# Kernel optimization log

Measured on AMD Instinct MI355X. Metric: run time of the kernel, lower is better.

Reference implementation:

```python
import jax, jax.numpy as jnp
import numpy as np

B, N, H, DH, E, D_IN = 2, 2048, 8, 32, 65536, 256
O = H * DH
SCALE = float(np.sqrt(DH))


def setup_inputs() -> dict:
    key = jax.random.key(0)
    ks = jax.random.split(key, 8)
    rng = np.random.default_rng(0)
    x = jax.random.normal(ks[0], (B, N, D_IN), jnp.float32)
    adj = jax.random.uniform(ks[1], (B, N, N), jnp.float32)
    # unique edges per graph so scatter-add matches torch advanced-index +=
    flat = np.stack([rng.choice(N * N, size=E, replace=False) for _ in range(B)])
    edge_index = jnp.asarray(np.stack([flat // N, flat % N], axis=1), jnp.int32)  # [B,2,E]
    edge_attr = jax.random.normal(ks[2], (B, E, H), jnp.float32)
    mask = jnp.ones((B, N), dtype=bool)
    qkv_w = jax.random.normal(ks[3], (D_IN, 3 * O), jnp.float32) / np.sqrt(D_IN)
    qkv_b = jnp.zeros((3 * O,), jnp.float32)
    e_w1 = jax.random.normal(ks[4], (H, H), jnp.float32) / np.sqrt(H)
    e_b1 = jnp.zeros((H,), jnp.float32)
    e_w2 = jax.random.normal(ks[5], (H, H), jnp.float32) / np.sqrt(H)
    e_b2 = jnp.zeros((H,), jnp.float32)
    shifts = jnp.asarray(np.linspace(0.1, 0.8, H), jnp.float32).reshape(1, H, 1, 1)
    widths = jnp.full((1, H, 1, 1), 0.5, jnp.float32)
    self_loop_W = jnp.asarray(1.0 / DH + rng.uniform(0, 1, H), jnp.float32).reshape(1, H, 1, 1)
    return dict(x=x, adj=adj, edge_attr=edge_attr, qkv_w=qkv_w, qkv_b=qkv_b,
                e_w1=e_w1, e_b1=e_b1, e_w2=e_w2, e_b2=e_b2,
                shifts=shifts, widths=widths, self_loop_W=self_loop_W,
                edge_index=edge_index, mask=mask)


def reference(x, adj, edge_attr, qkv_w, qkv_b, e_w1, e_b1, e_w2, e_b2,
              shifts, widths, self_loop_W, edge_index, mask):
    Bq, Nq = x.shape[0], x.shape[1]
    # qkv projection -> [3,B,H,N,DH]
    qkv = (x @ qkv_w + qkv_b).reshape(Bq, Nq, 3, H, DH)
    qkv = jnp.transpose(qkv, (2, 0, 3, 1, 4))
    Q, K, V = qkv[0], qkv[1], qkv[2]
    # edge FFN applied twice (eval mode: noise/dropout are identity)
    def ffn(e):
        return jax.nn.relu(e @ e_w1 + e_b1) @ e_w2 + e_b2
    ea = ffn(ffn(edge_attr))                      # [B,E,H]
    ea = jnp.transpose(ea, (0, 2, 1))             # [B,H,E]
    # scores + learned moire adjacency bias
    scores = jnp.einsum('bhqd,bhkd->bhqk', Q, K) / SCALE
    moire = jnp.exp(-((adj[:, None] - shifts) ** 2) / (2.0 * widths ** 2))  # gaussian focus
    moire = jnp.clip(moire, 1e-6, None)
    s = scores + jnp.log(moire)                   # [B,H,N,N]
    # scatter edge features into score matrix
    u = edge_index[:, 0, :]                        # [B,E]
    v = edge_index[:, 1, :]
    bi = jnp.arange(Bq)[:, None, None]
    hi = jnp.arange(H)[None, :, None]
    s = s.at[bi, hi, u[:, None, :], v[:, None, :]].add(ea)
    # self-loop diagonal bias (non-trainable)
    s = s + jnp.eye(Nq, dtype=s.dtype)[None, None] * self_loop_W
    # mask and softmax
    m2 = mask[:, None, :] & mask[:, :, None]       # [B,N,N]
    s = jnp.where(m2[:, None], s, jnp.asarray(-1e6, s.dtype))
    attn = jax.nn.softmax(s, axis=-1)
    out = jnp.einsum('bhqk,bhkd->bhqd', attn, V)
    return jnp.transpose(out, (0, 2, 1, 3)).reshape(Bq, Nq, O)
```

## Files before the change

kernel.cpp:

```cpp
#include <hip/hip_runtime.h>

#define B_ 2
#define N_ 2048
#define H_ 8
#define DH_ 32
#define E_ 65536
#define DIN_ 256
#define KT 256
#define PAD 4
#define ECAP 32
#define INV_SCALE 0.17677669529663687f
#define LOGMIN -13.815510557964274f

typedef short bf16x8 __attribute__((ext_vector_type(8)));
typedef float floatx4 __attribute__((ext_vector_type(4)));

__device__ __forceinline__ unsigned short f2b(float f){
  union { float f; unsigned int u; } v; v.f = f;
  return (unsigned short)((v.u + 0x7fffu + ((v.u >> 16) & 1u)) >> 16);
}
__device__ __forceinline__ bf16x8 f8_to_bf(const float* p){
  float4 a = *(const float4*)p, b = *(const float4*)(p + 4);
  bf16x8 r;
  r[0] = (short)f2b(a.x); r[1] = (short)f2b(a.y); r[2] = (short)f2b(a.z); r[3] = (short)f2b(a.w);
  r[4] = (short)f2b(b.x); r[5] = (short)f2b(b.y); r[6] = (short)f2b(b.z); r[7] = (short)f2b(b.w);
  return r;
}

__global__ __launch_bounds__(256) void prep_kernel(
    const float* __restrict__ eattr,
    const float* __restrict__ w1, const float* __restrict__ b1,
    const float* __restrict__ w2, const float* __restrict__ b2,
    float* __restrict__ ea,
    const int* __restrict__ ei, int* __restrict__ cnt, unsigned int* __restrict__ pck,
    const float* __restrict__ w, unsigned short* __restrict__ wT)
{
  int bb = blockIdx.x, tid = threadIdx.x;
  if (bb < 512){
    __shared__ float W1[64], W2[64], Bv1[8], Bv2[8];
    if (tid < 64){ W1[tid] = w1[tid]; W2[tid] = w2[tid]; }
    if (tid < 8){ Bv1[tid] = b1[tid]; Bv2[tid] = b2[tid]; }
    __syncthreads();
    int gid = bb * 256 + tid;
    const float* ep = eattr + (size_t)gid * 8;
    float cur[8];
#pragma unroll
    for (int i = 0; i < 8; ++i) cur[i] = ep[i];
#pragma unroll
    for (int pass = 0; pass < 2; ++pass){
      float t[8];
#pragma unroll
      for (int j = 0; j < 8; ++j){
        float s = Bv1[j];
#pragma unroll
        for (int i = 0; i < 8; ++i) s += cur[i] * W1[i * 8 + j];
        t[j] = fmaxf(s, 0.f);
      }
#pragma unroll
      for (int j = 0; j < 8; ++j){
        float s = Bv2[j];
#pragma unroll
        for (int i = 0; i < 8; ++i) s += t[i] * W2[i * 8 + j];
        cur[j] = s;
      }
    }
    float* op = ea + (size_t)gid * 8;
#pragma unroll
    for (int j = 0; j < 8; ++j) op[j] = cur[j];
  } else if (bb < 1024){
    int gid = (bb - 512) * 256 + tid;
    int b = gid >> 16, e = gid & (E_ - 1);
    int u = ei[(size_t)b * 2 * E_ + e];
    int v = ei[(size_t)b * 2 * E_ + E_ + e];
    int bucket = ((b << 11) + u) * 8 + (v >> 8);
    int slot = atomicAdd(&cnt[bucket], 1);
    if (slot < ECAP) pck[(size_t)bucket * ECAP + slot] = ((unsigned int)e << 11) | (unsigned int)v;
  } else {
    int k = bb - 1024;
    for (int c = tid; c < 768; c += 256)
      wT[(size_t)c * 256 + k] = f2b(w[(size_t)k * 768 + c]);
  }
}

__global__ __launch_bounds__(256) void qkv_kernel(
    const float* __restrict__ x, const unsigned short* __restrict__ wT,
    const float* __restrict__ bias,
    unsigned short* __restrict__ Qb, unsigned short* __restrict__ Kb, unsigned short* __restrict__ Vt)
{
  int tid = threadIdx.x;
  int wave = tid >> 6, lane = tid & 63, m = lane & 15, quad = lane >> 4;
  int rowbase = blockIdx.x * 16;
  int colbase = blockIdx.y * 64 + wave * 16;
  floatx4 acc = {0.f, 0.f, 0.f, 0.f};
#pragma unroll
  for (int kb = 0; kb < 8; ++kb){
    bf16x8 af = f8_to_bf(x + (size_t)(rowbase + m) * DIN_ + kb * 32 + quad * 8);
    bf16x8 bf = *(const bf16x8*)(wT + (size_t)(colbase + m) * DIN_ + kb * 32 + quad * 8);
    acc = __builtin_amdgcn_mfma_f32_16x16x32_bf16(af, bf, acc, 0, 0, 0);
  }
  int ccol = colbase + m;
  int which = ccol >> 8, hh = (ccol >> 5) & 7, dh = ccol & 31;
  float bv = bias[ccol];
#pragma unroll
  for (int r = 0; r < 4; ++r){
    int row = rowbase + quad * 4 + r;
    int bidx = row >> 11, n = row & (N_ - 1);
    float val = acc[r] + bv;
    size_t bh = (size_t)(bidx * H_ + hh);
    if (which == 0)      Qb[(bh * N_ + n) * DH_ + dh] = f2b(val * INV_SCALE);
    else if (which == 1) Kb[(bh * N_ + n) * DH_ + dh] = f2b(val);
    else                 Vt[(bh * DH_ + dh) * N_ + n] = f2b(val);
  }
}

__global__ __launch_bounds__(256) void attn_kernel(
    const unsigned short* __restrict__ Qb, const unsigned short* __restrict__ Kb,
    const unsigned short* __restrict__ Vt, const float* __restrict__ adj,
    const float* __restrict__ ea, const int* __restrict__ cnt, const unsigned int* __restrict__ pck,
    const float* __restrict__ shifts, const float* __restrict__ widths,
    const float* __restrict__ selfW, float* __restrict__ out)
{
  __shared__ float S[16][KT + PAD];
  __shared__ float mpart[4][16];
  __shared__ float mrowW[4][16];
  __shared__ float arowW[4][16];
  __shared__ float lfin[4][16];

  int bid = blockIdx.x;
  int qt = bid & 127, h = (bid >> 7) & 7, b = bid >> 10;
  int qbase = qt * 16;
  int tid = threadIdx.x, wave = tid >> 6, lane = tid & 63, m = lane & 15, quad = lane >> 4;
  float shift_h = shifts[h];
  float w_h = widths[h];
  float i2w_h = 1.f / (2.f * w_h * w_h);
  float selfW_h = selfW[h];
  size_t krow = (size_t)(b * H_ + h) * N_;
  size_t vrow = (size_t)(b * H_ + h) * DH_;
  bf16x8 qfrag = *(const bf16x8*)(Qb + (krow + qbase + m) * DH_ + quad * 8);

  float mcur = -1e30f;
  float lcur = 0.f;
  floatx4 oacc0 = {0.f, 0.f, 0.f, 0.f};
  floatx4 oacc1 = {0.f, 0.f, 0.f, 0.f};

  for (int kt = 0; kt < N_ / KT; ++kt){
    int k0 = kt * KT;
    bool diagtile = (k0 == (qbase & ~(KT - 1)));
#pragma unroll
    for (int s = 0; s < 4; ++s){
      int colofs = wave * 64 + s * 16;
      bf16x8 kf = *(const bf16x8*)(Kb + (krow + k0 + colofs + m) * DH_ + quad * 8);
      floatx4 acc = {0.f, 0.f, 0.f, 0.f};
      acc = __builtin_amdgcn_mfma_f32_16x16x32_bf16(qfrag, kf, acc, 0, 0, 0);
      int t = colofs + m - (qbase - k0);
#pragma unroll
      for (int r = 0; r < 4; ++r){
        float v = acc[r];
        if (diagtile && t == quad * 4 + r) v += selfW_h;
        S[quad * 4 + r][colofs + m] = v;
      }
    }
    __syncthreads();
#pragma unroll
    for (int ii = 0; ii < 4; ++ii){
      int i = tid + ii * 256;
      int r = i >> 6, c4 = (i & 63) << 2;
      float4 av = *(const float4*)(adj + ((size_t)b * N_ + qbase + r) * N_ + k0 + c4);
      float4* sp = (float4*)&S[r][c4];
      float4 sv = *sp;
      float d;
      d = av.x - shift_h; sv.x += fmaxf(-d * d * i2w_h, LOGMIN);
      d = av.y - shift_h; sv.y += fmaxf(-d * d * i2w_h, LOGMIN);
      d = av.z - shift_h; sv.z += fmaxf(-d * d * i2w_h, LOGMIN);
      d = av.w - shift_h; sv.w += fmaxf(-d * d * i2w_h, LOGMIN);
      *sp = sv;
    }
    __syncthreads();
#pragma unroll
    for (int ii = 0; ii < 2; ++ii){
      int i = tid + ii * 256;
      int r = i >> 5, slot = i & (ECAP - 1);
      int bucket = (b * N_ + qbase + r) * 8 + kt;
      int nb = cnt[bucket]; nb = nb > ECAP ? ECAP : nb;
      if (slot < nb){
        unsigned int p = pck[(size_t)bucket * ECAP + slot];
        int vv = (int)(p & (N_ - 1));
        int e  = (int)(p >> 11);
        S[r][vv - k0] += ea[((size_t)b * E_ + e) * H_ + h];
      }
    }
    __syncthreads();
    const float* sp0 = &S[m][wave * 64 + quad * 8];
    float4 s00 = *(const float4*)(sp0);
    float4 s01 = *(const float4*)(sp0 + 4);
    float4 s10 = *(const float4*)(sp0 + 32);
    float4 s11 = *(const float4*)(sp0 + 36);
    bf16x8 vf00 = *(const bf16x8*)(Vt + (vrow + m) * N_      + k0 + wave * 64 + quad * 8);
    bf16x8 vf01 = *(const bf16x8*)(Vt + (vrow + 16 + m) * N_ + k0 + wave * 64 + quad * 8);
    bf16x8 vf10 = *(const bf16x8*)(Vt + (vrow + m) * N_      + k0 + wave * 64 + 32 + quad * 8);
    bf16x8 vf11 = *(const bf16x8*)(Vt + (vrow + 16 + m) * N_ + k0 + wave * 64 + 32 + quad * 8);
    float lm = fmaxf(fmaxf(fmaxf(s00.x, s00.y), fmaxf(s00.z, s00.w)),
                     fmaxf(fmaxf(s01.x, s01.y), fmaxf(s01.z, s01.w)));
    lm = fmaxf(lm, fmaxf(fmaxf(fmaxf(s10.x, s10.y), fmaxf(s10.z, s10.w)),
                         fmaxf(fmaxf(s11.x, s11.y), fmaxf(s11.z, s11.w))));
    lm = fmaxf(lm, __shfl_xor(lm, 16));
    lm = fmaxf(lm, __shfl_xor(lm, 32));
    if (quad == 0) mpart[wave][m] = lm;
    __syncthreads();
    if (lane < 16){
      float tmax = fmaxf(fmaxf(mpart[0][lane], mpart[1][lane]),
                         fmaxf(mpart[2][lane], mpart[3][lane]));
      float mnew = fmaxf(mcur, tmax);
      float al = __expf(mcur - mnew);
      mcur = mnew;
      mrowW[wave][lane] = mnew;
      arowW[wave][lane] = al;
    }
    __threadfence_block();
    float mr  = mrowW[wave][m];
    float alA = arowW[wave][m];
    float4 aq = *(const float4*)&arowW[wave][quad * 4];
    oacc0[0] *= aq.x; oacc0[1] *= aq.y; oacc0[2] *= aq.z; oacc0[3] *= aq.w;
    oacc1[0] *= aq.x; oacc1[1] *= aq.y; oacc1[2] *= aq.z; oacc1[3] *= aq.w;
    float ps = 0.f, p;
    bf16x8 pf;
    p = __expf(s00.x - mr); ps += p; pf[0] = (short)f2b(p);
    p = __expf(s00.y - mr); ps += p; pf[1] = (short)f2b(p);
    p = __expf(s00.z - mr); ps += p; pf[2] = (short)f2b(p);
    p = __expf(s00.w - mr); ps += p; pf[3] = (short)f2b(p);
    p = __expf(s01.x - mr); ps += p; pf[4] = (short)f2b(p);
    p = __expf(s01.y - mr); ps += p; pf[5] = (short)f2b(p);
    p = __expf(s01.z - mr); ps += p; pf[6] = (short)f2b(p);
    p = __expf(s01.w - mr); ps += p; pf[7] = (short)f2b(p);
    oacc0 = __builtin_amdgcn_mfma_f32_16x16x32_bf16(pf, vf00, oacc0, 0, 0, 0);
    oacc1 = __builtin_amdgcn_mfma_f32_16x16x32_bf16(pf, vf01, oacc1, 0, 0, 0);
    p = __expf(s10.x - mr); ps += p; pf[0] = (short)f2b(p);
    p = __expf(s10.y - mr); ps += p; pf[1] = (short)f2b(p);
    p = __expf(s10.z - mr); ps += p; pf[2] = (short)f2b(p);
    p = __expf(s10.w - mr); ps += p; pf[3] = (short)f2b(p);
    p = __expf(s11.x - mr); ps += p; pf[4] = (short)f2b(p);
    p = __expf(s11.y - mr); ps += p; pf[5] = (short)f2b(p);
    p = __expf(s11.z - mr); ps += p; pf[6] = (short)f2b(p);
    p = __expf(s11.w - mr); ps += p; pf[7] = (short)f2b(p);
    oacc0 = __builtin_amdgcn_mfma_f32_16x16x32_bf16(pf, vf10, oacc0, 0, 0, 0);
    oacc1 = __builtin_amdgcn_mfma_f32_16x16x32_bf16(pf, vf11, oacc1, 0, 0, 0);
    ps += __shfl_xor(ps, 16);
    ps += __shfl_xor(ps, 32);
    lcur = lcur * alA + ps;
  }

  float* Op = &S[0][0];
#pragma unroll
  for (int r = 0; r < 4; ++r){
    Op[(wave * 16 + quad * 4 + r) * 32 + m]      = oacc0[r];
    Op[(wave * 16 + quad * 4 + r) * 32 + 16 + m] = oacc1[r];
  }
  if (lane < 16) lfin[wave][lane] = lcur;
  __syncthreads();
#pragma unroll
  for (int ii = 0; ii < 2; ++ii){
    int i = tid + ii * 256;
    int r = i >> 5, d = i & 31;
    float o = Op[r * 32 + d] + Op[(16 + r) * 32 + d] + Op[(32 + r) * 32 + d] + Op[(48 + r) * 32 + d];
    float l = lfin[0][r] + lfin[1][r] + lfin[2][r] + lfin[3][r];
    out[((size_t)b * N_ + qbase + r) * (H_ * DH_) + h * DH_ + d] = o / l;
  }
}

extern "C" void kernel_launch(void* const* d_in, const int* in_sizes, int n_in,
                              void* d_out, int out_size, void* d_ws, size_t ws_size,
                              hipStream_t stream)
{
  const float* x      = (const float*)d_in[0];
  const float* adj    = (const float*)d_in[1];
  const float* eattr  = (const float*)d_in[2];
  const float* qkvw   = (const float*)d_in[3];
  const float* qkvb   = (const float*)d_in[4];
  const float* ew1    = (const float*)d_in[5];
  const float* eb1    = (const float*)d_in[6];
  const float* ew2    = (const float*)d_in[7];
  const float* eb2    = (const float*)d_in[8];
  const float* shifts = (const float*)d_in[9];
  const float* widths = (const float*)d_in[10];
  const float* selfW  = (const float*)d_in[11];
  const int*   ei     = (const int*)d_in[12];
  float* out = (float*)d_out;

  char* ws = (char*)d_ws;
  unsigned short* Qb  = (unsigned short*)(ws);
  unsigned short* Kb  = (unsigned short*)(ws + ((size_t)2 << 20));
  unsigned short* Vt  = (unsigned short*)(ws + ((size_t)4 << 20));
  unsigned short* wT  = (unsigned short*)(ws + ((size_t)6 << 20));
  float*          ea  = (float*)(ws + ((size_t)7 << 20));
  int*            cnt = (int*)(ws + ((size_t)11 << 20));
  unsigned int*  pck  = (unsigned int*)(ws + ((size_t)12 << 20));

  hipMemsetAsync(cnt, 0, (size_t)B_ * N_ * 8 * sizeof(int), stream);
  hipLaunchKernelGGL(prep_kernel, dim3(1280), dim3(256), 0, stream,
                     eattr, ew1, eb1, ew2, eb2, ea, ei, cnt, pck, qkvw, wT);
  hipLaunchKernelGGL(qkv_kernel, dim3(256, 12), dim3(256), 0, stream, x, wT, qkvb, Qb, Kb, Vt);
  hipLaunchKernelGGL(attn_kernel, dim3(B_ * H_ * (N_ / 16)), dim3(256), 0, stream,
                     Qb, Kb, Vt, adj, ea, cnt, pck, shifts, widths, selfW, out);
}
```

Baseline: 238.1 us.

## Double query tile per block, fuse adj bias into registers, use exp2 softmax

Each attention block now handles 32 query rows instead of 16, so every K and V fragment load feeds two MFMAs and the grid is halved. The Gaussian adjacency bias is computed in registers, read straight from global memory during the softmax pass, instead of in a separate shared-memory pass, which removes one barrier per tile. The softmax moves to base 2: log2(e) is folded into Q's scale, the edge features and the self-loop weight, so exp2f replaces __expf. Probabilities are packed to bf16 by truncation with a perm instruction, and the row sums use the same truncated values. The cost is more registers and shared memory per block, fewer blocks in flight, and slightly different rounding.

```diff
diff --git a/kernel.cpp b/kernel.cpp
--- a/kernel.cpp
+++ b/kernel.cpp
@@ -9,8 +9,9 @@
 #define KT 256
 #define PAD 4
 #define ECAP 32
-#define INV_SCALE 0.17677669529663687f
-#define LOGMIN -13.815510557964274f
+#define LOG2E 1.4426950408889634f
+#define QSCALE 0.2550349880f
+#define LOGMIN2 -19.931568569324174f
 
 typedef short bf16x8 __attribute__((ext_vector_type(8)));
 typedef float floatx4 __attribute__((ext_vector_type(4)));
@@ -25,6 +26,15 @@
   r[0] = (short)f2b(a.x); r[1] = (short)f2b(a.y); r[2] = (short)f2b(a.z); r[3] = (short)f2b(a.w);
   r[4] = (short)f2b(b.x); r[5] = (short)f2b(b.y); r[6] = (short)f2b(b.z); r[7] = (short)f2b(b.w);
   return r;
+}
+__device__ __forceinline__ unsigned int fbits(float f){
+  union { float f; unsigned int u; } v; v.f = f; return v.u;
+}
+__device__ __forceinline__ float ftrunc16(float f){
+  union { unsigned int u; float f; } v; v.u = fbits(f) & 0xffff0000u; return v.f;
+}
+__device__ __forceinline__ unsigned int pack_trunc(float lo, float hi){
+  return __builtin_amdgcn_perm(fbits(hi), fbits(lo), 0x07060302u);
 }
 
 __global__ __launch_bounds__(256) void prep_kernel(
@@ -66,7 +76,7 @@
     }
     float* op = ea + (size_t)gid * 8;
 #pragma unroll
-    for (int j = 0; j < 8; ++j) op[j] = cur[j];
+    for (int j = 0; j < 8; ++j) op[j] = cur[j] * LOG2E;
   } else if (bb < 1024){
     int gid = (bb - 512) * 256 + tid;
     int b = gid >> 16, e = gid & (E_ - 1);
@@ -107,7 +117,7 @@
     int bidx = row >> 11, n = row & (N_ - 1);
     float val = acc[r] + bv;
     size_t bh = (size_t)(bidx * H_ + hh);
-    if (which == 0)      Qb[(bh * N_ + n) * DH_ + dh] = f2b(val * INV_SCALE);
+    if (which == 0)      Qb[(bh * N_ + n) * DH_ + dh] = f2b(val * QSCALE);
     else if (which == 1) Kb[(bh * N_ + n) * DH_ + dh] = f2b(val);
     else                 Vt[(bh * DH_ + dh) * N_ + n] = f2b(val);
   }
@@ -120,64 +130,56 @@
     const float* __restrict__ shifts, const float* __restrict__ widths,
     const float* __restrict__ selfW, float* __restrict__ out)
 {
-  __shared__ float S[16][KT + PAD];
-  __shared__ float mpart[4][16];
-  __shared__ float mrowW[4][16];
-  __shared__ float arowW[4][16];
-  __shared__ float lfin[4][16];
+  __shared__ float S[32][KT + PAD];
+  __shared__ float mpart[4][32];
+  __shared__ float mrowW[4][32];
+  __shared__ float arowW[4][32];
+  __shared__ float lfin[4][32];
 
   int bid = blockIdx.x;
-  int qt = bid & 127, h = (bid >> 7) & 7, b = bid >> 10;
-  int qbase = qt * 16;
+  int qt = bid & 63, h = (bid >> 6) & 7, b = bid >> 9;
+  int qbase = qt * 32;
   int tid = threadIdx.x, wave = tid >> 6, lane = tid & 63, m = lane & 15, quad = lane >> 4;
   float shift_h = shifts[h];
   float w_h = widths[h];
-  float i2w_h = 1.f / (2.f * w_h * w_h);
-  float selfW_h = selfW[h];
+  float ni = -LOG2E / (2.f * w_h * w_h);
+  float selfW_h = selfW[h] * LOG2E;
   size_t krow = (size_t)(b * H_ + h) * N_;
   size_t vrow = (size_t)(b * H_ + h) * DH_;
-  bf16x8 qfrag = *(const bf16x8*)(Qb + (krow + qbase + m) * DH_ + quad * 8);
-
-  float mcur = -1e30f;
-  float lcur = 0.f;
-  floatx4 oacc0 = {0.f, 0.f, 0.f, 0.f};
-  floatx4 oacc1 = {0.f, 0.f, 0.f, 0.f};
+  bf16x8 qfrag0 = *(const bf16x8*)(Qb + (krow + qbase + m) * DH_ + quad * 8);
+  bf16x8 qfrag1 = *(const bf16x8*)(Qb + (krow + qbase + 16 + m) * DH_ + quad * 8);
+
+  float mcurA = -1e30f, mcurB = -1e30f;
+  float lcurA = 0.f, lcurB = 0.f;
+  floatx4 oA0 = {0,0,0,0}, oA1 = {0,0,0,0}, oB0 = {0,0,0,0}, oB1 = {0,0,0,0};
+
+  int c0 = wave * 64 + quad * 8;
+  int dqk = 0;
 
   for (int kt = 0; kt < N_ / KT; ++kt){
     int k0 = kt * KT;
     bool diagtile = (k0 == (qbase & ~(KT - 1)));
+    dqk = qbase - k0;
 #pragma unroll
     for (int s = 0; s < 4; ++s){
       int colofs = wave * 64 + s * 16;
       bf16x8 kf = *(const bf16x8*)(Kb + (krow + k0 + colofs + m) * DH_ + quad * 8);
-      floatx4 acc = {0.f, 0.f, 0.f, 0.f};
-      acc = __builtin_amdgcn_mfma_f32_16x16x32_bf16(qfrag, kf, acc, 0, 0, 0);
-      int t = colofs + m - (qbase - k0);
+      floatx4 aA = {0,0,0,0}, aB = {0,0,0,0};
+      aA = __builtin_amdgcn_mfma_f32_16x16x32_bf16(qfrag0, kf, aA, 0, 0, 0);
+      aB = __builtin_amdgcn_mfma_f32_16x16x32_bf16(qfrag1, kf, aB, 0, 0, 0);
+      int t = colofs + m - dqk;
 #pragma unroll
       for (int r = 0; r < 4; ++r){
-        float v = acc[r];
-        if (diagtile && t == quad * 4 + r) v += selfW_h;
-        S[quad * 4 + r][colofs + m] = v;
+        float vA = aA[r], vB = aB[r];
+        if (diagtile && t == quad * 4 + r)      vA += selfW_h;
+        if (diagtile && t == 16 + quad * 4 + r) vB += selfW_h;
+        S[quad * 4 + r][colofs + m] = vA;
+        S[16 + quad * 4 + r][colofs + m] = vB;
       }
     }
     __syncthreads();
 #pragma unroll
     for (int ii = 0; ii < 4; ++ii){
-      int i = tid + ii * 256;
-      int r = i >> 6, c4 = (i & 63) << 2;
-      float4 av = *(const float4*)(adj + ((size_t)b * N_ + qbase + r) * N_ + k0 + c4);
-      float4* sp = (float4*)&S[r][c4];
-      float4 sv = *sp;
-      float d;
-      d = av.x - shift_h; sv.x += fmaxf(-d * d * i2w_h, LOGMIN);
-      d = av.y - shift_h; sv.y += fmaxf(-d * d * i2w_h, LOGMIN);
-      d = av.z - shift_h; sv.z += fmaxf(-d * d * i2w_h, LOGMIN);
-      d = av.w - shift_h; sv.w += fmaxf(-d * d * i2w_h, LOGMIN);
-      *sp = sv;
-    }
-    __syncthreads();
-#pragma unroll
-    for (int ii = 0; ii < 2; ++ii){
       int i = tid + ii * 256;
       int r = i >> 5, slot = i & (ECAP - 1);
       int bucket = (b * N_ + qbase + r) * 8 + kt;
@@ -190,78 +192,137 @@
       }
     }
     __syncthreads();
-    const float* sp0 = &S[m][wave * 64 + quad * 8];
-    float4 s00 = *(const float4*)(sp0);
-    float4 s01 = *(const float4*)(sp0 + 4);
-    float4 s10 = *(const float4*)(sp0 + 32);
-    float4 s11 = *(const float4*)(sp0 + 36);
-    bf16x8 vf00 = *(const bf16x8*)(Vt + (vrow + m) * N_      + k0 + wave * 64 + quad * 8);
-    bf16x8 vf01 = *(const bf16x8*)(Vt + (vrow + 16 + m) * N_ + k0 + wave * 64 + quad * 8);
-    bf16x8 vf10 = *(const bf16x8*)(Vt + (vrow + m) * N_      + k0 + wave * 64 + 32 + quad * 8);
-    bf16x8 vf11 = *(const bf16x8*)(Vt + (vrow + 16 + m) * N_ + k0 + wave * 64 + 32 + quad * 8);
-    float lm = fmaxf(fmaxf(fmaxf(s00.x, s00.y), fmaxf(s00.z, s00.w)),
-                     fmaxf(fmaxf(s01.x, s01.y), fmaxf(s01.z, s01.w)));
-    lm = fmaxf(lm, fmaxf(fmaxf(fmaxf(s10.x, s10.y), fmaxf(s10.z, s10.w)),
-                         fmaxf(fmaxf(s11.x, s11.y), fmaxf(s11.z, s11.w))));
-    lm = fmaxf(lm, __shfl_xor(lm, 16));
-    lm = fmaxf(lm, __shfl_xor(lm, 32));
-    if (quad == 0) mpart[wave][m] = lm;
+    const float* SrA = &S[m][c0];
+    const float* SrB = &S[16 + m][c0];
+    const float* ArA = adj + ((size_t)b * N_ + qbase + m) * N_ + k0 + c0;
+    const float* ArB = adj + ((size_t)b * N_ + qbase + 16 + m) * N_ + k0 + c0;
+    float4 sA0 = *(const float4*)(SrA),      sA1 = *(const float4*)(SrA + 4);
+    float4 sA2 = *(const float4*)(SrA + 32), sA3 = *(const float4*)(SrA + 36);
+    float4 sB0 = *(const float4*)(SrB),      sB1 = *(const float4*)(SrB + 4);
+    float4 sB2 = *(const float4*)(SrB + 32), sB3 = *(const float4*)(SrB + 36);
+    {
+      float4 a0 = *(const float4*)(ArA),      a1 = *(const float4*)(ArA + 4);
+      float4 a2 = *(const float4*)(ArA + 32), a3 = *(const float4*)(ArA + 36);
+      float d;
+      d = a0.x - shift_h; sA0.x += fmaxf(d * d * ni, LOGMIN2);
+      d = a0.y - shift_h; sA0.y += fmaxf(d * d * ni, LOGMIN2);
+      d = a0.z - shift_h; sA0.z += fmaxf(d * d * ni, LOGMIN2);
+      d = a0.w - shift_h; sA0.w += fmaxf(d * d * ni, LOGMIN2);
+      d = a1.x - shift_h; sA1.x += fmaxf(d * d * ni, LOGMIN2);
+      d = a1.y - shift_h; sA1.y += fmaxf(d * d * ni, LOGMIN2);
+      d = a1.z - shift_h; sA1.z += fmaxf(d * d * ni, LOGMIN2);
+      d = a1.w - shift_h; sA1.w += fmaxf(d * d * ni, LOGMIN2);
+      d = a2.x - shift_h; sA2.x += fmaxf(d * d * ni, LOGMIN2);
+      d = a2.y - shift_h; sA2.y += fmaxf(d * d * ni, LOGMIN2);
+      d = a2.z - shift_h; sA2.z += fmaxf(d * d * ni, LOGMIN2);
+      d = a2.w - shift_h; sA2.w += fmaxf(d * d * ni, LOGMIN2);
+      d = a3.x - shift_h; sA3.x += fmaxf(d * d * ni, LOGMIN2);
+      d = a3.y - shift_h; sA3.y += fmaxf(d * d * ni, LOGMIN2);
+      d = a3.z - shift_h; sA3.z += fmaxf(d * d * ni, LOGMIN2);
+      d = a3.w - shift_h; sA3.w += fmaxf(d * d * ni, LOGMIN2);
+      a0 = *(const float4*)(ArB);      a1 = *(const float4*)(ArB + 4);
+      a2 = *(const float4*)(ArB + 32); a3 = *(const float4*)(ArB + 36);
+      d = a0.x - shift_h; sB0.x += fmaxf(d * d * ni, LOGMIN2);
+      d = a0.y - shift_h; sB0.y += fmaxf(d * d * ni, LOGMIN2);
+      d = a0.z - shift_h; sB0.z += fmaxf(d * d * ni, LOGMIN2);
+      d = a0.w - shift_h; sB0.w += fmaxf(d * d * ni, LOGMIN2);
+      d = a1.x - shift_h; sB1.x += fmaxf(d * d * ni, LOGMIN2);
+      d = a1.y - shift_h; sB1.y += fmaxf(d * d * ni, LOGMIN2);
+      d = a1.z - shift_h; sB1.z += fmaxf(d * d * ni, LOGMIN2);
+      d = a1.w - shift_h; sB1.w += fmaxf(d * d * ni, LOGMIN2);
+      d = a2.x - shift_h; sB2.x += fmaxf(d * d * ni, LOGMIN2);
+      d = a2.y - shift_h; sB2.y += fmaxf(d * d * ni, LOGMIN2);
+      d = a2.z - shift_h; sB2.z += fmaxf(d * d * ni, LOGMIN2);
+      d = a2.w - shift_h; sB2.w += fmaxf(d * d * ni, LOGMIN2);
+      d = a3.x - shift_h; sB3.x += fmaxf(d * d * ni, LOGMIN2);
+      d = a3.y - shift_h; sB3.y += fmaxf(d * d * ni, LOGMIN2);
+      d = a3.z - shift_h; sB3.z += fmaxf(d * d * ni, LOGMIN2);
+      d = a3.w - shift_h; sB3.w += fmaxf(d * d * ni, LOGMIN2);
+    }
+    float lmA = fmaxf(fmaxf(fmaxf(sA0.x, sA0.y), fmaxf(sA0.z, sA0.w)),
+                      fmaxf(fmaxf(sA1.x, sA1.y), fmaxf(sA1.z, sA1.w)));
+    lmA = fmaxf(lmA, fmaxf(fmaxf(fmaxf(sA2.x, sA2.y), fmaxf(sA2.z, sA2.w)),
+                           fmaxf(fmaxf(sA3.x, sA3.y), fmaxf(sA3.z, sA3.w))));
+    float lmB = fmaxf(fmaxf(fmaxf(sB0.x, sB0.y), fmaxf(sB0.z, sB0.w)),
+                      fmaxf(fmaxf(sB1.x, sB1.y), fmaxf(sB1.z, sB1.w)));
+    lmB = fmaxf(lmB, fmaxf(fmaxf(fmaxf(sB2.x, sB2.y), fmaxf(sB2.z, sB2.w)),
+                           fmaxf(fmaxf(sB3.x, sB3.y), fmaxf(sB3.z, sB3.w))));
+    lmA = fmaxf(lmA, __shfl_xor(lmA, 16)); lmA = fmaxf(lmA, __shfl_xor(lmA, 32));
+    lmB = fmaxf(lmB, __shfl_xor(lmB, 16)); lmB = fmaxf(lmB, __shfl_xor(lmB, 32));
+    if (quad == 0){ mpart[wave][m] = lmA; mpart[wave][16 + m] = lmB; }
     __syncthreads();
-    if (lane < 16){
+    if (lane < 32){
+      float mcur = (lane < 16) ? mcurA : mcurB;
       float tmax = fmaxf(fmaxf(mpart[0][lane], mpart[1][lane]),
                          fmaxf(mpart[2][lane], mpart[3][lane]));
       float mnew = fmaxf(mcur, tmax);
-      float al = __expf(mcur - mnew);
-      mcur = mnew;
       mrowW[wave][lane] = mnew;
-      arowW[wave][lane] = al;
+      arowW[wave][lane] = exp2f(mcur - mnew);
+      if (lane < 16) mcurA = mnew; else mcurB = mnew;
     }
     __threadfence_block();
-    float mr  = mrowW[wave][m];
-    float alA = arowW[wave][m];
-    float4 aq = *(const float4*)&arowW[wave][quad * 4];
-    oacc0[0] *= aq.x; oacc0[1] *= aq.y; oacc0[2] *= aq.z; oacc0[3] *= aq.w;
-    oacc1[0] *= aq.x; oacc1[1] *= aq.y; oacc1[2] *= aq.z; oacc1[3] *= aq.w;
-    float ps = 0.f, p;
-    bf16x8 pf;
-    p = __expf(s00.x - mr); ps += p; pf[0] = (short)f2b(p);
-    p = __expf(s00.y - mr); ps += p; pf[1] = (short)f2b(p);
-    p = __expf(s00.z - mr); ps += p; pf[2] = (short)f2b(p);
-    p = __expf(s00.w - mr); ps += p; pf[3] = (short)f2b(p);
-    p = __expf(s01.x - mr); ps += p; pf[4] = (short)f2b(p);
-    p = __expf(s01.y - mr); ps += p; pf[5] = (short)f2b(p);
-    p = __expf(s01.z - mr); ps += p; pf[6] = (short)f2b(p);
-    p = __expf(s01.w - mr); ps += p; pf[7] = (short)f2b(p);
-    oacc0 = __builtin_amdgcn_mfma_f32_16x16x32_bf16(pf, vf00, oacc0, 0, 0, 0);
-    oacc1 = __builtin_amdgcn_mfma_f32_16x16x32_bf16(pf, vf01, oacc1, 0, 0, 0);
-    p = __expf(s10.x - mr); ps += p; pf[0] = (short)f2b(p);
-    p = __expf(s10.y - mr); ps += p; pf[1] = (short)f2b(p);
-    p = __expf(s10.z - mr); ps += p; pf[2] = (short)f2b(p);
-    p = __expf(s10.w - mr); ps += p; pf[3] = (short)f2b(p);
-    p = __expf(s11.x - mr); ps += p; pf[4] = (short)f2b(p);
-    p = __expf(s11.y - mr); ps += p; pf[5] = (short)f2b(p);
-    p = __expf(s11.z - mr); ps += p; pf[6] = (short)f2b(p);
-    p = __expf(s11.w - mr); ps += p; pf[7] = (short)f2b(p);
-    oacc0 = __builtin_amdgcn_mfma_f32_16x16x32_bf16(pf, vf10, oacc0, 0, 0, 0);
-    oacc1 = __builtin_amdgcn_mfma_f32_16x16x32_bf16(pf, vf11, oacc1, 0, 0, 0);
-    ps += __shfl_xor(ps, 16);
-    ps += __shfl_xor(ps, 32);
-    lcur = lcur * alA + ps;
+    mcurA = mrowW[wave][m];
+    mcurB = mrowW[wave][16 + m];
+    float mrA = mcurA, mrB = mcurB;
+    float alA = arowW[wave][m], alB = arowW[wave][16 + m];
+    float4 aqA = *(const float4*)&arowW[wave][quad * 4];
+    float4 aqB = *(const float4*)&arowW[wave][16 + quad * 4];
+    oA0[0] *= aqA.x; oA0[1] *= aqA.y; oA0[2] *= aqA.z; oA0[3] *= aqA.w;
+    oA1[0] *= aqA.x; oA1[1] *= aqA.y; oA1[2] *= aqA.z; oA1[3] *= aqA.w;
+    oB0[0] *= aqB.x; oB0[1] *= aqB.y; oB0[2] *= aqB.z; oB0[3] *= aqB.w;
+    oB1[0] *= aqB.x; oB1[1] *= aqB.y; oB1[2] *= aqB.z; oB1[3] *= aqB.w;
+    bf16x8 vf00 = *(const bf16x8*)(Vt + (vrow + m) * N_      + k0 + c0);
+    bf16x8 vf01 = *(const bf16x8*)(Vt + (vrow + 16 + m) * N_ + k0 + c0);
+    bf16x8 vf10 = *(const bf16x8*)(Vt + (vrow + m) * N_      + k0 + c0 + 32);
+    bf16x8 vf11 = *(const bf16x8*)(Vt + (vrow + 16 + m) * N_ + k0 + c0 + 32);
+    float psA = 0.f, psB = 0.f;
+    union { bf16x8 v; unsigned int u[4]; } pf;
+    float p0, p1;
+    p0 = exp2f(sA0.x - mrA); p1 = exp2f(sA0.y - mrA); psA += ftrunc16(p0) + ftrunc16(p1); pf.u[0] = pack_trunc(p0, p1);
+    p0 = exp2f(sA0.z - mrA); p1 = exp2f(sA0.w - mrA); psA += ftrunc16(p0) + ftrunc16(p1); pf.u[1] = pack_trunc(p0, p1);
+    p0 = exp2f(sA1.x - mrA); p1 = exp2f(sA1.y - mrA); psA += ftrunc16(p0) + ftrunc16(p1); pf.u[2] = pack_trunc(p0, p1);
+    p0 = exp2f(sA1.z - mrA); p1 = exp2f(sA1.w - mrA); psA += ftrunc16(p0) + ftrunc16(p1); pf.u[3] = pack_trunc(p0, p1);
+    oA0 = __builtin_amdgcn_mfma_f32_16x16x32_bf16(pf.v, vf00, oA0, 0, 0, 0);
+    oA1 = __builtin_amdgcn_mfma_f32_16x16x32_bf16(pf.v, vf01, oA1, 0, 0, 0);
+    p0 = exp2f(sA2.x - mrA); p1 = exp2f(sA2.y - mrA); psA += ftrunc16(p0) + ftrunc16(p1); pf.u[0] = pack_trunc(p0, p1);
+    p0 = exp2f(sA2.z - mrA); p1 = exp2f(sA2.w - mrA); psA += ftrunc16(p0) + ftrunc16(p1); pf.u[1] = pack_trunc(p0, p1);
+    p0 = exp2f(sA3.x - mrA); p1 = exp2f(sA3.y - mrA); psA += ftrunc16(p0) + ftrunc16(p1); pf.u[2] = pack_trunc(p0, p1);
+    p0 = exp2f(sA3.z - mrA); p1 = exp2f(sA3.w - mrA); psA += ftrunc16(p0) + ftrunc16(p1); pf.u[3] = pack_trunc(p0, p1);
+    oA0 = __builtin_amdgcn_mfma_f32_16x16x32_bf16(pf.v, vf10, oA0, 0, 0, 0);
+    oA1 = __builtin_amdgcn_mfma_f32_16x16x32_bf16(pf.v, vf11, oA1, 0, 0, 0);
+    p0 = exp2f(sB0.x - mrB); p1 = exp2f(sB0.y - mrB); psB += ftrunc16(p0) + ftrunc16(p1); pf.u[0] = pack_trunc(p0, p1);
+    p0 = exp2f(sB0.z - mrB); p1 = exp2f(sB0.w - mrB); psB += ftrunc16(p0) + ftrunc16(p1); pf.u[1] = pack_trunc(p0, p1);
+    p0 = exp2f(sB1.x - mrB); p1 = exp2f(sB1.y - mrB); psB += ftrunc16(p0) + ftrunc16(p1); pf.u[2] = pack_trunc(p0, p1);
+    p0 = exp2f(sB1.z - mrB); p1 = exp2f(sB1.w - mrB); psB += ftrunc16(p0) + ftrunc16(p1); pf.u[3] = pack_trunc(p0, p1);
+    oB0 = __builtin_amdgcn_mfma_f32_16x16x32_bf16(pf.v, vf00, oB0, 0, 0, 0);
+    oB1 = __builtin_amdgcn_mfma_f32_16x16x32_bf16(pf.v, vf01, oB1, 0, 0, 0);
+    p0 = exp2f(sB2.x - mrB); p1 = exp2f(sB2.y - mrB); psB += ftrunc16(p0) + ftrunc16(p1); pf.u[0] = pack_trunc(p0, p1);
+    p0 = exp2f(sB2.z - mrB); p1 = exp2f(sB2.w - mrB); psB += ftrunc16(p0) + ftrunc16(p1); pf.u[1] = pack_trunc(p0, p1);
+    p0 = exp2f(sB3.x - mrB); p1 = exp2f(sB3.y - mrB); psB += ftrunc16(p0) + ftrunc16(p1); pf.u[2] = pack_trunc(p0, p1);
+    p0 = exp2f(sB3.z - mrB); p1 = exp2f(sB3.w - mrB); psB += ftrunc16(p0) + ftrunc16(p1); pf.u[3] = pack_trunc(p0, p1);
+    oB0 = __builtin_amdgcn_mfma_f32_16x16x32_bf16(pf.v, vf10, oB0, 0, 0, 0);
+    oB1 = __builtin_amdgcn_mfma_f32_16x16x32_bf16(pf.v, vf11, oB1, 0, 0, 0);
+    psA += __shfl_xor(psA, 16); psA += __shfl_xor(psA, 32);
+    psB += __shfl_xor(psB, 16); psB += __shfl_xor(psB, 32);
+    lcurA = lcurA * alA + psA;
+    lcurB = lcurB * alB + psB;
   }
 
   float* Op = &S[0][0];
 #pragma unroll
   for (int r = 0; r < 4; ++r){
-    Op[(wave * 16 + quad * 4 + r) * 32 + m]      = oacc0[r];
-    Op[(wave * 16 + quad * 4 + r) * 32 + 16 + m] = oacc1[r];
-  }
-  if (lane < 16) lfin[wave][lane] = lcur;
+    Op[(wave * 32 + quad * 4 + r) * 32 + m]           = oA0[r];
+    Op[(wave * 32 + quad * 4 + r) * 32 + 16 + m]      = oA1[r];
+    Op[(wave * 32 + 16 + quad * 4 + r) * 32 + m]      = oB0[r];
+    Op[(wave * 32 + 16 + quad * 4 + r) * 32 + 16 + m] = oB1[r];
+  }
+  if (lane < 16){ lfin[wave][m] = lcurA; lfin[wave][16 + m] = lcurB; }
   __syncthreads();
 #pragma unroll
-  for (int ii = 0; ii < 2; ++ii){
+  for (int ii = 0; ii < 4; ++ii){
     int i = tid + ii * 256;
     int r = i >> 5, d = i & 31;
-    float o = Op[r * 32 + d] + Op[(16 + r) * 32 + d] + Op[(32 + r) * 32 + d] + Op[(48 + r) * 32 + d];
+    float o = Op[r * 32 + d] + Op[(32 + r) * 32 + d] + Op[(64 + r) * 32 + d] + Op[(96 + r) * 32 + d];
     float l = lfin[0][r] + lfin[1][r] + lfin[2][r] + lfin[3][r];
     out[((size_t)b * N_ + qbase + r) * (H_ * DH_) + h * DH_ + d] = o / l;
   }
@@ -299,6 +360,6 @@
   hipLaunchKernelGGL(prep_kernel, dim3(1280), dim3(256), 0, stream,
                      eattr, ew1, eb1, ew2, eb2, ea, ei, cnt, pck, qkvw, wT);
   hipLaunchKernelGGL(qkv_kernel, dim3(256, 12), dim3(256), 0, stream, x, wT, qkvb, Qb, Kb, Vt);
-  hipLaunchKernelGGL(attn_kernel, dim3(B_ * H_ * (N_ / 16)), dim3(256), 0, stream,
+  hipLaunchKernelGGL(attn_kernel, dim3(B_ * H_ * (N_ / 32)), dim3(256), 0, stream,
                      Qb, Kb, Vt, adj, ea, cnt, pck, shifts, widths, selfW, out);
 }
```

Measured after the change: 268.7 us. +12.9%, slower.

## Drop online-softmax max tracking and block barriers; use exp2 with folded log2e scaling

Applied to the files above, without the earlier changes.

Removes the running row-max and rescaling from the attention loop, relying on scores being small enough to exponentiate directly. log2(e) is folded into the Q scale, the edge features, the self-loop bias and the Gaussian coefficient so exp2f can be used. Each wave now writes and reads only its own 64-column slice of the shared score tile, so the per-tile __syncthreads calls go away; adj is read and fused directly into the QK^T write, and the edge scatter is filtered per wave. Probabilities are packed to bf16 by truncation with a perm instruction, and the row sum uses the same truncated values. Skipping max subtraction risks overflow if scores grow large.

```diff
diff --git a/kernel.cpp b/kernel.cpp
--- a/kernel.cpp
+++ b/kernel.cpp
@@ -9,8 +9,9 @@
 #define KT 256
 #define PAD 4
 #define ECAP 32
-#define INV_SCALE 0.17677669529663687f
-#define LOGMIN -13.815510557964274f
+#define LOG2E 1.4426950408889634f
+#define QSCALE 0.2550349880f
+#define LOGMIN2 -19.931568569324174f
 
 typedef short bf16x8 __attribute__((ext_vector_type(8)));
 typedef float floatx4 __attribute__((ext_vector_type(4)));
@@ -25,6 +26,15 @@
   r[0] = (short)f2b(a.x); r[1] = (short)f2b(a.y); r[2] = (short)f2b(a.z); r[3] = (short)f2b(a.w);
   r[4] = (short)f2b(b.x); r[5] = (short)f2b(b.y); r[6] = (short)f2b(b.z); r[7] = (short)f2b(b.w);
   return r;
+}
+__device__ __forceinline__ unsigned int fbits(float f){
+  union { float f; unsigned int u; } v; v.f = f; return v.u;
+}
+__device__ __forceinline__ float ftrunc16(float f){
+  union { unsigned int u; float f; } v; v.u = fbits(f) & 0xffff0000u; return v.f;
+}
+__device__ __forceinline__ unsigned int pack_trunc(float lo, float hi){
+  return __builtin_amdgcn_perm(fbits(hi), fbits(lo), 0x07060302u);
 }
 
 __global__ __launch_bounds__(256) void prep_kernel(
@@ -66,7 +76,7 @@
     }
     float* op = ea + (size_t)gid * 8;
 #pragma unroll
-    for (int j = 0; j < 8; ++j) op[j] = cur[j];
+    for (int j = 0; j < 8; ++j) op[j] = cur[j] * LOG2E;
   } else if (bb < 1024){
     int gid = (bb - 512) * 256 + tid;
     int b = gid >> 16, e = gid & (E_ - 1);
@@ -107,7 +117,7 @@
     int bidx = row >> 11, n = row & (N_ - 1);
     float val = acc[r] + bv;
     size_t bh = (size_t)(bidx * H_ + hh);
-    if (which == 0)      Qb[(bh * N_ + n) * DH_ + dh] = f2b(val * INV_SCALE);
+    if (which == 0)      Qb[(bh * N_ + n) * DH_ + dh] = f2b(val * QSCALE);
     else if (which == 1) Kb[(bh * N_ + n) * DH_ + dh] = f2b(val);
     else                 Vt[(bh * DH_ + dh) * N_ + n] = f2b(val);
   }
@@ -121,9 +131,6 @@
     const float* __restrict__ selfW, float* __restrict__ out)
 {
   __shared__ float S[16][KT + PAD];
-  __shared__ float mpart[4][16];
-  __shared__ float mrowW[4][16];
-  __shared__ float arowW[4][16];
   __shared__ float lfin[4][16];
 
   int bid = blockIdx.x;
@@ -132,130 +139,90 @@
   int tid = threadIdx.x, wave = tid >> 6, lane = tid & 63, m = lane & 15, quad = lane >> 4;
   float shift_h = shifts[h];
   float w_h = widths[h];
-  float i2w_h = 1.f / (2.f * w_h * w_h);
-  float selfW_h = selfW[h];
+  float ni = -LOG2E / (2.f * w_h * w_h);
+  float selfW_h = selfW[h] * LOG2E;
   size_t krow = (size_t)(b * H_ + h) * N_;
   size_t vrow = (size_t)(b * H_ + h) * DH_;
   bf16x8 qfrag = *(const bf16x8*)(Qb + (krow + qbase + m) * DH_ + quad * 8);
 
-  float mcur = -1e30f;
   float lcur = 0.f;
-  floatx4 oacc0 = {0.f, 0.f, 0.f, 0.f};
-  floatx4 oacc1 = {0.f, 0.f, 0.f, 0.f};
+  floatx4 o0 = {0,0,0,0}, o1 = {0,0,0,0};
+
+  int c0 = wave * 64 + quad * 8;
+  int rowbase8 = (b * N_ + qbase) * 8;
+  int diagkt = qbase >> 8;
+  const float* adjq = adj + ((size_t)b * N_ + qbase) * N_;
+  size_t bE8 = (size_t)b * E_ * 8;
 
   for (int kt = 0; kt < N_ / KT; ++kt){
     int k0 = kt * KT;
-    bool diagtile = (k0 == (qbase & ~(KT - 1)));
 #pragma unroll
     for (int s = 0; s < 4; ++s){
       int colofs = wave * 64 + s * 16;
       bf16x8 kf = *(const bf16x8*)(Kb + (krow + k0 + colofs + m) * DH_ + quad * 8);
-      floatx4 acc = {0.f, 0.f, 0.f, 0.f};
+      floatx4 acc = {0,0,0,0};
       acc = __builtin_amdgcn_mfma_f32_16x16x32_bf16(qfrag, kf, acc, 0, 0, 0);
-      int t = colofs + m - (qbase - k0);
 #pragma unroll
       for (int r = 0; r < 4; ++r){
-        float v = acc[r];
-        if (diagtile && t == quad * 4 + r) v += selfW_h;
-        S[quad * 4 + r][colofs + m] = v;
-      }
-    }
-    __syncthreads();
-#pragma unroll
-    for (int ii = 0; ii < 4; ++ii){
-      int i = tid + ii * 256;
-      int r = i >> 6, c4 = (i & 63) << 2;
-      float4 av = *(const float4*)(adj + ((size_t)b * N_ + qbase + r) * N_ + k0 + c4);
-      float4* sp = (float4*)&S[r][c4];
-      float4 sv = *sp;
-      float d;
-      d = av.x - shift_h; sv.x += fmaxf(-d * d * i2w_h, LOGMIN);
-      d = av.y - shift_h; sv.y += fmaxf(-d * d * i2w_h, LOGMIN);
-      d = av.z - shift_h; sv.z += fmaxf(-d * d * i2w_h, LOGMIN);
-      d = av.w - shift_h; sv.w += fmaxf(-d * d * i2w_h, LOGMIN);
-      *sp = sv;
-    }
-    __syncthreads();
-#pragma unroll
-    for (int ii = 0; ii < 2; ++ii){
-      int i = tid + ii * 256;
-      int r = i >> 5, slot = i & (ECAP - 1);
-      int bucket = (b * N_ + qbase + r) * 8 + kt;
+        float a = adjq[(size_t)(quad * 4 + r) * N_ + k0 + colofs + m];
+        float d = a - shift_h;
+        S[quad * 4 + r][colofs + m] = acc[r] + fmaxf(d * d * ni, LOGMIN2);
+      }
+    }
+    if (kt == diagkt && quad == 0){
+      int cl = (qbase - k0) + m;
+      if ((cl >> 6) == wave) S[m][cl] += selfW_h;
+    }
+#pragma unroll
+    for (int it = 0; it < 8; ++it){
+      int i = lane + it * 64;
+      int r = i >> 5, slot = i & 31;
+      int bucket = rowbase8 + r * 8 + kt;
       int nb = cnt[bucket]; nb = nb > ECAP ? ECAP : nb;
       if (slot < nb){
         unsigned int p = pck[(size_t)bucket * ECAP + slot];
-        int vv = (int)(p & (N_ - 1));
-        int e  = (int)(p >> 11);
-        S[r][vv - k0] += ea[((size_t)b * E_ + e) * H_ + h];
-      }
-    }
-    __syncthreads();
-    const float* sp0 = &S[m][wave * 64 + quad * 8];
-    float4 s00 = *(const float4*)(sp0);
-    float4 s01 = *(const float4*)(sp0 + 4);
-    float4 s10 = *(const float4*)(sp0 + 32);
-    float4 s11 = *(const float4*)(sp0 + 36);
-    bf16x8 vf00 = *(const bf16x8*)(Vt + (vrow + m) * N_      + k0 + wave * 64 + quad * 8);
-    bf16x8 vf01 = *(const bf16x8*)(Vt + (vrow + 16 + m) * N_ + k0 + wave * 64 + quad * 8);
-    bf16x8 vf10 = *(const bf16x8*)(Vt + (vrow + m) * N_      + k0 + wave * 64 + 32 + quad * 8);
-    bf16x8 vf11 = *(const bf16x8*)(Vt + (vrow + 16 + m) * N_ + k0 + wave * 64 + 32 + quad * 8);
-    float lm = fmaxf(fmaxf(fmaxf(s00.x, s00.y), fmaxf(s00.z, s00.w)),
-                     fmaxf(fmaxf(s01.x, s01.y), fmaxf(s01.z, s01.w)));
-    lm = fmaxf(lm, fmaxf(fmaxf(fmaxf(s10.x, s10.y), fmaxf(s10.z, s10.w)),
-                         fmaxf(fmaxf(s11.x, s11.y), fmaxf(s11.z, s11.w))));
-    lm = fmaxf(lm, __shfl_xor(lm, 16));
-    lm = fmaxf(lm, __shfl_xor(lm, 32));
-    if (quad == 0) mpart[wave][m] = lm;
-    __syncthreads();
-    if (lane < 16){
-      float tmax = fmaxf(fmaxf(mpart[0][lane], mpart[1][lane]),
-                         fmaxf(mpart[2][lane], mpart[3][lane]));
-      float mnew = fmaxf(mcur, tmax);
-      float al = __expf(mcur - mnew);
-      mcur = mnew;
-      mrowW[wave][lane] = mnew;
-      arowW[wave][lane] = al;
-    }
-    __threadfence_block();
-    float mr  = mrowW[wave][m];
-    float alA = arowW[wave][m];
-    float4 aq = *(const float4*)&arowW[wave][quad * 4];
-    oacc0[0] *= aq.x; oacc0[1] *= aq.y; oacc0[2] *= aq.z; oacc0[3] *= aq.w;
-    oacc1[0] *= aq.x; oacc1[1] *= aq.y; oacc1[2] *= aq.z; oacc1[3] *= aq.w;
-    float ps = 0.f, p;
-    bf16x8 pf;
-    p = __expf(s00.x - mr); ps += p; pf[0] = (short)f2b(p);
-    p = __expf(s00.y - mr); ps += p; pf[1] = (short)f2b(p);
-    p = __expf(s00.z - mr); ps += p; pf[2] = (short)f2b(p);
-    p = __expf(s00.w - mr); ps += p; pf[3] = (short)f2b(p);
-    p = __expf(s01.x - mr); ps += p; pf[4] = (short)f2b(p);
-    p = __expf(s01.y - mr); ps += p; pf[5] = (short)f2b(p);
-    p = __expf(s01.z - mr); ps += p; pf[6] = (short)f2b(p);
-    p = __expf(s01.w - mr); ps += p; pf[7] = (short)f2b(p);
-    oacc0 = __builtin_amdgcn_mfma_f32_16x16x32_bf16(pf, vf00, oacc0, 0, 0, 0);
-    oacc1 = __builtin_amdgcn_mfma_f32_16x16x32_bf16(pf, vf01, oacc1, 0, 0, 0);
-    p = __expf(s10.x - mr); ps += p; pf[0] = (short)f2b(p);
-    p = __expf(s10.y - mr); ps += p; pf[1] = (short)f2b(p);
-    p = __expf(s10.z - mr); ps += p; pf[2] = (short)f2b(p);
-    p = __expf(s10.w - mr); ps += p; pf[3] = (short)f2b(p);
-    p = __expf(s11.x - mr); ps += p; pf[4] = (short)f2b(p);
-    p = __expf(s11.y - mr); ps += p; pf[5] = (short)f2b(p);
-    p = __expf(s11.z - mr); ps += p; pf[6] = (short)f2b(p);
-    p = __expf(s11.w - mr); ps += p; pf[7] = (short)f2b(p);
-    oacc0 = __builtin_amdgcn_mfma_f32_16x16x32_bf16(pf, vf10, oacc0, 0, 0, 0);
-    oacc1 = __builtin_amdgcn_mfma_f32_16x16x32_bf16(pf, vf11, oacc1, 0, 0, 0);
+        int rel = (int)(p & (N_ - 1)) - k0 - wave * 64;
+        if ((unsigned)rel < 64u){
+          int e = (int)(p >> 11);
+          S[r][wave * 64 + rel] += ea[bE8 + (size_t)e * 8 + h];
+        }
+      }
+    }
+    bf16x8 vf0 = *(const bf16x8*)(Vt + (vrow + m) * N_      + k0 + c0);
+    bf16x8 vf1 = *(const bf16x8*)(Vt + (vrow + 16 + m) * N_ + k0 + c0);
+    bf16x8 vf2 = *(const bf16x8*)(Vt + (vrow + m) * N_      + k0 + c0 + 32);
+    bf16x8 vf3 = *(const bf16x8*)(Vt + (vrow + 16 + m) * N_ + k0 + c0 + 32);
+    const float* sp = &S[m][c0];
+    float4 s0 = *(const float4*)(sp),      s1 = *(const float4*)(sp + 4);
+    float4 s2 = *(const float4*)(sp + 32), s3 = *(const float4*)(sp + 36);
+    float ps = 0.f, p0, p1;
+    union { bf16x8 v; unsigned int u[4]; } pf;
+    p0 = exp2f(s0.x); p1 = exp2f(s0.y); ps += ftrunc16(p0) + ftrunc16(p1); pf.u[0] = pack_trunc(p0, p1);
+    p0 = exp2f(s0.z); p1 = exp2f(s0.w); ps += ftrunc16(p0) + ftrunc16(p1); pf.u[1] = pack_trunc(p0, p1);
+    p0 = exp2f(s1.x); p1 = exp2f(s1.y); ps += ftrunc16(p0) + ftrunc16(p1); pf.u[2] = pack_trunc(p0, p1);
+    p0 = exp2f(s1.z); p1 = exp2f(s1.w); ps += ftrunc16(p0) + ftrunc16(p1); pf.u[3] = pack_trunc(p0, p1);
+    o0 = __builtin_amdgcn_mfma_f32_16x16x32_bf16(pf.v, vf0, o0, 0, 0, 0);
+    o1 = __builtin_amdgcn_mfma_f32_16x16x32_bf16(pf.v, vf1, o1, 0, 0, 0);
+    p0 = exp2f(s2.x); p1 = exp2f(s2.y); ps += ftrunc16(p0) + ftrunc16(p1); pf.u[0] = pack_trunc(p0, p1);
+    p0 = exp2f(s2.z); p1 = exp2f(s2.w); ps += ftrunc16(p0) + ftrunc16(p1); pf.u[1] = pack_trunc(p0, p1);
+    p0 = exp2f(s3.x); p1 = exp2f(s3.y); ps += ftrunc16(p0) + ftrunc16(p1); pf.u[2] = pack_trunc(p0, p1);
+    p0 = exp2f(s3.z); p1 = exp2f(s3.w); ps += ftrunc16(p0) + ftrunc16(p1); pf.u[3] = pack_trunc(p0, p1);
+    o0 = __builtin_amdgcn_mfma_f32_16x16x32_bf16(pf.v, vf2, o0, 0, 0, 0);
+    o1 = __builtin_amdgcn_mfma_f32_16x16x32_bf16(pf.v, vf3, o1, 0, 0, 0);
     ps += __shfl_xor(ps, 16);
     ps += __shfl_xor(ps, 32);
-    lcur = lcur * alA + ps;
-  }
+    lcur += ps;
+  }
+
+  __syncthreads();
 
   float* Op = &S[0][0];
 #pragma unroll
   for (int r = 0; r < 4; ++r){
-    Op[(wave * 16 + quad * 4 + r) * 32 + m]      = oacc0[r];
-    Op[(wave * 16 + quad * 4 + r) * 32 + 16 + m] = oacc1[r];
-  }
-  if (lane < 16) lfin[wave][lane] = lcur;
+    Op[(wave * 16 + quad * 4 + r) * 32 + m]      = o0[r];
+    Op[(wave * 16 + quad * 4 + r) * 32 + 16 + m] = o1[r];
+  }
+  if (lane < 16) lfin[wave][m] = lcur;
   __syncthreads();
 #pragma unroll
   for (int ii = 0; ii < 2; ++ii){
```

New measurement: 266.4 us. 1.12x slower.
